# Kernel tuning notes

Hardware: AMD Instinct MI355X
Metric: run time of the kernel (lower is better)

Reference implementation:

```python
import jax, jax.numpy as jnp
import numpy as np

N_ROWS = 100000   # sparse matrix rows (nodes)
N_COLS = 8192     # input feature dim
UNITS = 128
NNZ = 2000000     # ~20 nonzeros per row


def setup_inputs() -> dict:
    key = jax.random.key(0)
    k1, k2, k3, k4, k5 = jax.random.split(key, 5)
    vals = jax.random.normal(k1, (NNZ,), dtype=jnp.float32)
    rows = jax.random.randint(k2, (NNZ,), 0, N_ROWS, dtype=jnp.int32)
    cols = jax.random.randint(k3, (NNZ,), 0, N_COLS, dtype=jnp.int32)
    # GlorotUniform-style scale for W, matching the TF initializer statistics
    limit = jnp.sqrt(6.0 / (N_COLS + UNITS)).astype(jnp.float32)
    W = jax.random.uniform(k4, (N_COLS, UNITS), dtype=jnp.float32, minval=-limit, maxval=limit)
    b = jax.random.uniform(k5, (UNITS,), dtype=jnp.float32, minval=-limit, maxval=limit)
    return {"vals": vals, "rows": rows, "cols": cols, "W": W, "b": b, "num_rows": N_ROWS}


def reference(vals, rows, cols, W, b, num_rows):
    # sparse (COO) [num_rows, F] @ dense W [F, units]:
    # gather the W row for each nonzero, scale by the nonzero value,
    # then scatter-add into the output row -> segment_sum over `rows`.
    gathered = W[cols] * vals[:, None]            # [nnz, units]
    out = jax.ops.segment_sum(gathered, rows, num_segments=num_rows)  # [num_rows, units]
    return out + b                                 # bias add (use_bias=True)
```

## Files before the change

### kernel.cpp

```cpp
#include <hip/hip_runtime.h>
#include <hip/hip_fp16.h>


#define UNITS 128
#define SCAN_BLK 1024
#define BROW 98
#define CBROW 784
#define NCC 128
#define CCAP 17664
#define CH3 4096
#define SLOTS 40
#define OVF_CAP 256
#define SPILL_CAP 8192


__global__ __launch_bounds__(512, 8) void partition_kernel(
        const float* __restrict__ vals, const int* __restrict__ rows,
        const int* __restrict__ cols, const float* __restrict__ W,
        __half2* __restrict__ Wh, int* __restrict__ ccur,
        float2* __restrict__ sortedA, float2* __restrict__ spill,
        int nnz, int nbcc, int wn2) {
    __shared__ float2 sStage[CH3];
    __shared__ unsigned char sBkt[CH3];
    __shared__ int hist[NCC];
    __shared__ int gdelta[NCC];

    const int t = threadIdx.x;
    const int lane = t & 63;
    const int w = t >> 6;
    const int bb = blockIdx.x;

    {
        const float2* W2 = (const float2*)W;
        int stride = gridDim.x * 512;
        for (int i = bb * 512 + t; i < wn2; i += stride)
            Wh[i] = __float22half2_rn(W2[i]);
    }

    const int chunk0 = bb * CH3;
    int n = nnz - chunk0;
    if (n > CH3) n = CH3;

    if (t < NCC) hist[t] = 0;
    __syncthreads();

    int rbuf[8];
#pragma unroll
    for (int j = 0; j < 8; ++j) {
        int r = j * 512 + t;
        int rv = -1;
        if (r < n) {
            rv = rows[chunk0 + r];
            atomicAdd(&hist[rv / CBROW], 1);
        }
        rbuf[j] = rv;
    }
    __syncthreads();

    if (w == 0) {
        int a0 = hist[2 * lane], a1 = hist[2 * lane + 1];
        int ps = a0 + a1;
        int inc = ps;
#pragma unroll
        for (int o = 1; o < 64; o <<= 1) {
            int u = __shfl_up(inc, o);
            if (lane >= o) inc += u;
        }
        int excl = inc - ps;
        int s0 = 2 * lane, s1 = 2 * lane + 1;
        int g0 = (s0 < nbcc && a0 > 0) ? atomicAdd(&ccur[s0 * 16], a0) : 0;
        int g1 = (s1 < nbcc && a1 > 0) ? atomicAdd(&ccur[s1 * 16], a1) : 0;
        gdelta[s0] = s0 * CCAP + g0 - excl;
        gdelta[s1] = s1 * CCAP + g1 - (excl + a0);
        hist[s0] = excl;
        hist[s1] = excl + a0;
    }
    __syncthreads();

#pragma unroll
    for (int j = 0; j < 8; ++j) {
        int rv = rbuf[j];
        if (rv >= 0) {
            int r = j * 512 + t;
            int bkt = rv / CBROW;
            int rlo = rv - bkt * CBROW;
            int pos = atomicAdd(&hist[bkt], 1);
            float v = vals[chunk0 + r];
            int col = cols[chunk0 + r];
            sStage[pos] = make_float2(v, __int_as_float(col | (rlo << 13)));
            sBkt[pos] = (unsigned char)bkt;
        }
    }
    __syncthreads();

    int* spill_cnt = &ccur[NCC * 16];
    for (int s = t; s < n; s += 512) {
        float2 e = sStage[s];
        int bkt = sBkt[s];
        int dest = gdelta[bkt] + s;
        if (dest < (bkt + 1) * CCAP) {
            sortedA[dest] = e;
        } else {
            int sp = atomicAdd(spill_cnt, 1);
            if (sp < SPILL_CAP) {
                int pk = __float_as_int(e.y);
                int row = bkt * CBROW + (pk >> 13);
                spill[sp] = make_float2(e.x, __int_as_float((pk & 8191) | (row << 13)));
            }
        }
    }
}


__global__ __launch_bounds__(512, 8) void fused_sort_compute_kernel(
        const float2* __restrict__ A, const int* __restrict__ ccur,
        const __half2* __restrict__ Wh, const float* __restrict__ b,
        float* __restrict__ out, const float2* __restrict__ spill, int NR) {
    __shared__ float2 st[BROW * SLOTS];
    __shared__ float2 ovf[OVF_CAP];
    __shared__ int cnt_s[BROW + 6];
    __shared__ int ovf_n;
    __shared__ int spill_n;
    const int t = threadIdx.x;
    const int lane = t & 63;
    const int w = t >> 6;

    const int nwg = gridDim.x;
    const int orig = blockIdx.x;
    const int q = nwg >> 3, r8 = nwg & 7, xcd = orig & 7, idx = orig >> 3;
    const int f = (xcd < r8 ? xcd * (q + 1) : r8 * (q + 1) + (xcd - r8) * q) + idx;

    const int c = f >> 3, sb = f & 7;
    const int r0 = f * BROW;
    const int rlo0 = sb * BROW;
    const size_t base = (size_t)c * CCAP;
    int segn = ccur[c * 16];
    if (segn > CCAP) segn = CCAP;

    const float2 bias = ((const float2*)b)[lane];

    if (t < BROW + 6) cnt_s[t] = 0;
    if (t == 0) {
        ovf_n = 0;
        int sn = ccur[NCC * 16];
        spill_n = (sn > SPILL_CAP) ? SPILL_CAP : sn;
    }
    for (int i = t; i < BROW * SLOTS; i += 512)
        st[i] = make_float2(0.f, __int_as_float(0));
    __syncthreads();

    const float4* A4 = (const float4*)(A + base);
    const int seg2 = segn >> 1;
    for (int k2 = t; k2 < seg2; k2 += 512) {
        float4 qv = A4[k2];
        {
            int pk = __float_as_int(qv.y);
            unsigned rl = (unsigned)(pk >> 13) - rlo0;
            if (rl < BROW) {
                int p = atomicAdd(&cnt_s[rl], 1);
                if (p < SLOTS) st[rl * SLOTS + p] = make_float2(qv.x, __int_as_float(pk & 8191));
                else {
                    int qn = atomicAdd(&ovf_n, 1);
                    if (qn < OVF_CAP) ovf[qn] = make_float2(qv.x, __int_as_float((pk & 8191) | (rl << 13)));
                }
            }
        }
        {
            int pk = __float_as_int(qv.w);
            unsigned rl = (unsigned)(pk >> 13) - rlo0;
            if (rl < BROW) {
                int p = atomicAdd(&cnt_s[rl], 1);
                if (p < SLOTS) st[rl * SLOTS + p] = make_float2(qv.z, __int_as_float(pk & 8191));
                else {
                    int qn = atomicAdd(&ovf_n, 1);
                    if (qn < OVF_CAP) ovf[qn] = make_float2(qv.z, __int_as_float((pk & 8191) | (rl << 13)));
                }
            }
        }
    }
    if ((segn & 1) && t == 0) {
        float2 e = A[base + segn - 1];
        int pk = __float_as_int(e.y);
        unsigned rl = (unsigned)(pk >> 13) - rlo0;
        if (rl < BROW) {
            int p = atomicAdd(&cnt_s[rl], 1);
            if (p < SLOTS) st[rl * SLOTS + p] = make_float2(e.x, __int_as_float(pk & 8191));
            else {
                int qn = atomicAdd(&ovf_n, 1);
                if (qn < OVF_CAP) ovf[qn] = make_float2(e.x, __int_as_float((pk & 8191) | (rl << 13)));
            }
        }
    }
    __syncthreads();

    const int on = (ovf_n > OVF_CAP) ? OVF_CAP : ovf_n;
    const int sn = spill_n;
    for (int rA = w; rA < BROW; rA += 16) {
        const int rB = rA + 8;
        const bool hasB = (rB < BROW);
        int cA = cnt_s[rA]; if (cA > SLOTS) cA = SLOTS;
        int cB = 0;
        if (hasB) { cB = cnt_s[rB]; if (cB > SLOTS) cB = SLOTS; }
        const float2* sA = &st[rA * SLOTS];
        const float2* sB = &st[(hasB ? rB : rA) * SLOTS];
        int m = (cA > cB) ? cA : cB;
        m = (m + 3) & ~3;
        float axA0 = 0.f, ayA0 = 0.f, axA1 = 0.f, ayA1 = 0.f;
        float axB0 = 0.f, ayB0 = 0.f, axB1 = 0.f, ayB1 = 0.f;
        for (int k = 0; k < m; k += 4) {
            float2 a0 = sA[k], a1 = sA[k + 1], a2 = sA[k + 2], a3 = sA[k + 3];
            float2 b0 = sB[k], b1 = sB[k + 1], b2 = sB[k + 2], b3 = sB[k + 3];
            int ca0 = __float_as_int(a0.y) & 8191;
            int ca1 = __float_as_int(a1.y) & 8191;
            int ca2 = __float_as_int(a2.y) & 8191;
            int ca3 = __float_as_int(a3.y) & 8191;
            int cb0 = __float_as_int(b0.y) & 8191;
            int cb1 = __float_as_int(b1.y) & 8191;
            int cb2 = __float_as_int(b2.y) & 8191;
            int cb3 = __float_as_int(b3.y) & 8191;
            float2 wa0 = __half22float2(Wh[ca0 * 64 + lane]);
            float2 wa1 = __half22float2(Wh[ca1 * 64 + lane]);
            float2 wa2 = __half22float2(Wh[ca2 * 64 + lane]);
            float2 wa3 = __half22float2(Wh[ca3 * 64 + lane]);
            float2 wb0 = __half22float2(Wh[cb0 * 64 + lane]);
            float2 wb1 = __half22float2(Wh[cb1 * 64 + lane]);
            float2 wb2 = __half22float2(Wh[cb2 * 64 + lane]);
            float2 wb3 = __half22float2(Wh[cb3 * 64 + lane]);
            axA0 += a0.x * wa0.x; ayA0 += a0.x * wa0.y;
            axA1 += a1.x * wa1.x; ayA1 += a1.x * wa1.y;
            axA0 += a2.x * wa2.x; ayA0 += a2.x * wa2.y;
            axA1 += a3.x * wa3.x; ayA1 += a3.x * wa3.y;
            axB0 += b0.x * wb0.x; ayB0 += b0.x * wb0.y;
            axB1 += b1.x * wb1.x; ayB1 += b1.x * wb1.y;
            axB0 += b2.x * wb2.x; ayB0 += b2.x * wb2.y;
            axB1 += b3.x * wb3.x; ayB1 += b3.x * wb3.y;
        }
        {
            int grow = r0 + rA;
            if (grow < NR) {
                for (int q2 = 0; q2 < on; ++q2) {
                    float2 eo = ovf[q2];
                    int pk = __float_as_int(eo.y);
                    if ((pk >> 13) == rA) {
                        float2 wv = __half22float2(Wh[(pk & 8191) * 64 + lane]);
                        axA0 += eo.x * wv.x; ayA0 += eo.x * wv.y;
                    }
                }
                for (int s2 = 0; s2 < sn; ++s2) {
                    float2 es = spill[s2];
                    int pk = __float_as_int(es.y);
                    if ((pk >> 13) == grow) {
                        float2 wv = __half22float2(Wh[(pk & 8191) * 64 + lane]);
                        axA0 += es.x * wv.x; ayA0 += es.x * wv.y;
                    }
                }
                ((float2*)out)[(size_t)grow * 64 + lane] =
                    make_float2(axA0 + axA1 + bias.x, ayA0 + ayA1 + bias.y);
            }
        }
        if (hasB) {
            int grow = r0 + rB;
            if (grow < NR) {
                for (int q2 = 0; q2 < on; ++q2) {
                    float2 eo = ovf[q2];
                    int pk = __float_as_int(eo.y);
                    if ((pk >> 13) == rB) {
                        float2 wv = __half22float2(Wh[(pk & 8191) * 64 + lane]);
                        axB0 += eo.x * wv.x; ayB0 += eo.x * wv.y;
                    }
                }
                for (int s2 = 0; s2 < sn; ++s2) {
                    float2 es = spill[s2];
                    int pk = __float_as_int(es.y);
                    if ((pk >> 13) == grow) {
                        float2 wv = __half22float2(Wh[(pk & 8191) * 64 + lane]);
                        axB0 += es.x * wv.x; ayB0 += es.x * wv.y;
                    }
                }
                ((float2*)out)[(size_t)grow * 64 + lane] =
                    make_float2(axB0 + axB1 + bias.x, ayB0 + ayB1 + bias.y);
            }
        }
    }
}


__global__ void hist_kernel(const int* __restrict__ rows, int* __restrict__ counts, int nnz) {
    int i = blockIdx.x * blockDim.x + threadIdx.x;
    if (i < nnz) atomicAdd(&counts[rows[i]], 1);
}

__global__ void scan1_kernel(const int* __restrict__ counts, int* __restrict__ tmp,
                             int* __restrict__ bsums, int NR, int NS) {
    __shared__ int s[SCAN_BLK];
    int t = threadIdx.x;
    int i = blockIdx.x * SCAN_BLK + t;
    int x = (i < NR) ? counts[i] : 0;
    s[t] = x;
    __syncthreads();
    for (int off = 1; off < SCAN_BLK; off <<= 1) {
        int v = (t >= off) ? s[t - off] : 0;
        __syncthreads();
        s[t] += v;
        __syncthreads();
    }
    if (i < NS) tmp[i] = s[t] - x;
    if (t == SCAN_BLK - 1) bsums[blockIdx.x] = s[SCAN_BLK - 1];
}

__global__ void scan2_kernel(int* __restrict__ bsums, int nb) {
    if (threadIdx.x == 0 && blockIdx.x == 0) {
        int run = 0;
        for (int i = 0; i < nb; ++i) { int c = bsums[i]; bsums[i] = run; run += c; }
    }
}

__global__ void scan3_kernel(const int* __restrict__ tmp, const int* __restrict__ bsums,
                             int* __restrict__ row_start, int* __restrict__ cursor,
                             int NR, int NS) {
    int i = blockIdx.x * blockDim.x + threadIdx.x;
    if (i < NS) {
        int v = tmp[i] + bsums[i >> 10];
        row_start[i] = v;
        if (i < NR) cursor[i] = v;
    }
}

__global__ void scatter_sort_kernel(const float* __restrict__ vals, const int* __restrict__ rows,
                                    const int* __restrict__ cols, int* __restrict__ cursor,
                                    float2* __restrict__ sorted, int nnz) {
    int i = blockIdx.x * blockDim.x + threadIdx.x;
    if (i < nnz) {
        int r = rows[i];
        int p = atomicAdd(&cursor[r], 1);
        sorted[p] = make_float2(vals[i], __int_as_float(cols[i]));
    }
}

__global__ void compute_kernel(const float2* __restrict__ sorted, const int* __restrict__ row_start,
                               const float* __restrict__ W, const float* __restrict__ b,
                               float* __restrict__ out, int NR) {
    int lane = threadIdx.x & 63;
    int wv = threadIdx.x >> 6;
    int row = blockIdx.x * 4 + wv;
    if (row >= NR) return;
    int start = row_start[row];
    int end   = row_start[row + 1];
    const float2* W2 = (const float2*)W;
    float accx0 = 0.f, accy0 = 0.f, accx1 = 0.f, accy1 = 0.f;
    for (int base = start; base < end; base += 64) {
        int m = end - base;
        if (m > 64) m = 64;
        float2 p = make_float2(0.f, __int_as_float(0));
        if (lane < m) p = sorted[base + lane];
        int vi = __float_as_int(p.x);
        int ci = __float_as_int(p.y);
        int rounds = (m + 3) & ~3;
        for (int j = 0; j < rounds; j += 4) {
            float v0 = __int_as_float(__builtin_amdgcn_readlane(vi, j));
            int   c0 = __builtin_amdgcn_readlane(ci, j);
            float v1 = __int_as_float(__builtin_amdgcn_readlane(vi, j + 1));
            int   c1 = __builtin_amdgcn_readlane(ci, j + 1);
            float v2 = __int_as_float(__builtin_amdgcn_readlane(vi, j + 2));
            int   c2 = __builtin_amdgcn_readlane(ci, j + 2);
            float v3 = __int_as_float(__builtin_amdgcn_readlane(vi, j + 3));
            int   c3 = __builtin_amdgcn_readlane(ci, j + 3);
            float2 w0 = W2[c0 * 64 + lane];
            float2 w1 = W2[c1 * 64 + lane];
            float2 w2 = W2[c2 * 64 + lane];
            float2 w3 = W2[c3 * 64 + lane];
            accx0 += v0 * w0.x; accy0 += v0 * w0.y;
            accx1 += v1 * w1.x; accy1 += v1 * w1.y;
            accx0 += v2 * w2.x; accy0 += v2 * w2.y;
            accx1 += v3 * w3.x; accy1 += v3 * w3.y;
        }
    }
    float2 bb = ((const float2*)b)[lane];
    ((float2*)out)[(size_t)row * 64 + lane] =
        make_float2(accx0 + accx1 + bb.x, accy0 + accy1 + bb.y);
}


__global__ void init_bias_kernel(float* __restrict__ out, const float* __restrict__ b, int total4) {
    const float4* b4 = (const float4*)b;
    float4* out4 = (float4*)out;
    int stride = gridDim.x * blockDim.x;
    for (int j = blockIdx.x * blockDim.x + threadIdx.x; j < total4; j += stride)
        out4[j] = b4[j & 31];
}

__global__ void scatter_atomic_kernel(const float* __restrict__ vals, const int* __restrict__ rows,
                                      const int* __restrict__ cols, const float* __restrict__ W,
                                      float* __restrict__ out, int nnz) {
    long long idx = (long long)blockIdx.x * blockDim.x + threadIdx.x;
    int i = (int)(idx >> 5);
    int c = (int)(idx & 31);
    if (i >= nnz) return;
    int row = rows[i], col = cols[i];
    float v = vals[i];
    float4 w = ((const float4*)W)[col * 32 + c];
    float* o = out + (size_t)row * UNITS + (c << 2);
    atomicAdd(o + 0, v * w.x);
    atomicAdd(o + 1, v * w.y);
    atomicAdd(o + 2, v * w.z);
    atomicAdd(o + 3, v * w.w);
}

extern "C" void kernel_launch(void* const* d_in, const int* in_sizes, int n_in,
                              void* d_out, int out_size, void* d_ws, size_t ws_size,
                              hipStream_t stream) {
    const float* vals = (const float*)d_in[0];
    const int*   rows = (const int*)d_in[1];
    const int*   cols = (const int*)d_in[2];
    const float* W    = (const float*)d_in[3];
    const float* b    = (const float*)d_in[4];
    float* out = (float*)d_out;

    const int nnz = in_sizes[0];
    const int NW  = in_sizes[3];
    const int NR  = out_size / UNITS;
    const int NS  = NR + 1;
    const int NB  = (NS + SCAN_BLK - 1) / SCAN_BLK;
    const int nbf  = (NR + BROW - 1) / BROW;
    const int nbcc = (NR + CBROW - 1) / CBROW;

    auto align = [](size_t x) { return (x + 255) & ~(size_t)255; };

    size_t off_ccur    = 0;
    size_t off_wh      = align(off_ccur + (size_t)(NCC * 16 + 1) * 4);
    size_t off_sortedA = align(off_wh + (size_t)NW * 2);
    size_t off_spill   = align(off_sortedA + (size_t)NCC * CCAP * 8);
    size_t needed_full = off_spill + (size_t)SPILL_CAP * 8;

    size_t t2_counts   = 0;
    size_t t2_tmp      = align(t2_counts + (size_t)NR * 4);
    size_t t2_bsums    = align(t2_tmp    + (size_t)NS * 4);
    size_t t2_rowstart = align(t2_bsums  + (size_t)NB * 4);
    size_t t2_cursor   = align(t2_rowstart + (size_t)NS * 4);
    size_t t2_sorted   = align(t2_cursor + (size_t)NR * 4);
    size_t needed_r2   = t2_sorted + (size_t)nnz * 8;

    char* ws = (char*)d_ws;

    if (ws_size >= needed_full && nbcc >= 1 && nbcc <= NCC && NR >= 1) {
        int*     ccur    = (int*)(ws + off_ccur);
        __half2* Wh      = (__half2*)(ws + off_wh);
        float2*  sortedA = (float2*)(ws + off_sortedA);
        float2*  spill   = (float2*)(ws + off_spill);

        hipMemsetAsync(ccur, 0, (size_t)(NCC * 16 + 1) * 4, stream);
        {
            int grid = (nnz + CH3 - 1) / CH3;
            partition_kernel<<<grid, 512, 0, stream>>>(vals, rows, cols, W, Wh,
                                                       ccur, sortedA, spill,
                                                       nnz, nbcc, NW / 2);
        }
        fused_sort_compute_kernel<<<nbf, 512, 0, stream>>>(sortedA, ccur, Wh, b,
                                                           out, spill, NR);
    } else if (ws_size >= needed_r2) {
        int*    counts    = (int*)(ws + t2_counts);
        int*    tmp       = (int*)(ws + t2_tmp);
        int*    bsums     = (int*)(ws + t2_bsums);
        int*    row_start = (int*)(ws + t2_rowstart);
        int*    cursor    = (int*)(ws + t2_cursor);
        float2* sorted    = (float2*)(ws + t2_sorted);

        hipMemsetAsync(counts, 0, (size_t)NR * 4, stream);
        {
            int block = 256, grid = (nnz + block - 1) / block;
            hist_kernel<<<grid, block, 0, stream>>>(rows, counts, nnz);
        }
        scan1_kernel<<<NB, SCAN_BLK, 0, stream>>>(counts, tmp, bsums, NR, NS);
        scan2_kernel<<<1, 64, 0, stream>>>(bsums, NB);
        {
            int block = 256, grid = (NS + block - 1) / block;
            scan3_kernel<<<grid, block, 0, stream>>>(tmp, bsums, row_start, cursor, NR, NS);
        }
        {
            int block = 256, grid = (nnz + block - 1) / block;
            scatter_sort_kernel<<<grid, block, 0, stream>>>(vals, rows, cols, cursor, sorted, nnz);
        }
        {
            int grid = (NR + 3) / 4;
            compute_kernel<<<grid, 256, 0, stream>>>(sorted, row_start, W, b, out, NR);
        }
    } else {
        int total4 = out_size / 4;
        int block = 256;
        int grid = (total4 + block - 1) / block;
        init_bias_kernel<<<grid, block, 0, stream>>>(out, b, total4);
        long long total_threads = (long long)nnz * 32;
        long long g2 = (total_threads + block - 1) / block;
        scatter_atomic_kernel<<<(int)g2, block, 0, stream>>>(vals, rows, cols, W, out, nnz);
    }
}
```

Before: 156.5 us.

## Use fixed per-chunk bucket slots with sentinel padding instead of global atomic offsets

The partition kernel no longer reserves space in each bucket's segment with a global atomicAdd. Each (bucket, chunk) pair now owns a fixed slot range of PER entries in sortedA, and unused slots are filled with a sentinel row that the consumer ignores. Entries beyond PER go to a per-bucket overflow segment that the compute kernel also scans, and the global spill list with its per-row rescan is gone. This removes inter-block atomic contention and the spill scan, but the consumer now reads a padded segment (nch*PER entries per bucket, roughly double the real count) and the partition kernel writes extra padding.

Result: faster. 150.6 us (-3.8%).

```diff
diff --git a/kernel.cpp b/kernel.cpp
--- a/kernel.cpp
+++ b/kernel.cpp
@@ -7,23 +7,25 @@
 #define BROW 98
 #define CBROW 784
 #define NCC 128
-#define CCAP 17664
 #define CH3 4096
+#define PER 40
+#define OCAP 1024
 #define SLOTS 40
 #define OVF_CAP 256
-#define SPILL_CAP 8192
+#define SENT (1023 << 13)
 
 
 __global__ __launch_bounds__(512, 8) void partition_kernel(
         const float* __restrict__ vals, const int* __restrict__ rows,
         const int* __restrict__ cols, const float* __restrict__ W,
-        __half2* __restrict__ Wh, int* __restrict__ ccur,
-        float2* __restrict__ sortedA, float2* __restrict__ spill,
-        int nnz, int nbcc, int wn2) {
+        __half2* __restrict__ Wh, int* __restrict__ ocur,
+        float2* __restrict__ sortedA, float2* __restrict__ ovfseg,
+        int nnz, int nbcc, int nch, int wn2) {
     __shared__ float2 sStage[CH3];
     __shared__ unsigned char sBkt[CH3];
     __shared__ int hist[NCC];
-    __shared__ int gdelta[NCC];
+    __shared__ int excl[NCC];
+    __shared__ int cnt[NCC];
 
     const int t = threadIdx.x;
     const int lane = t & 63;
@@ -66,14 +68,10 @@
             int u = __shfl_up(inc, o);
             if (lane >= o) inc += u;
         }
-        int excl = inc - ps;
-        int s0 = 2 * lane, s1 = 2 * lane + 1;
-        int g0 = (s0 < nbcc && a0 > 0) ? atomicAdd(&ccur[s0 * 16], a0) : 0;
-        int g1 = (s1 < nbcc && a1 > 0) ? atomicAdd(&ccur[s1 * 16], a1) : 0;
-        gdelta[s0] = s0 * CCAP + g0 - excl;
-        gdelta[s1] = s1 * CCAP + g1 - (excl + a0);
-        hist[s0] = excl;
-        hist[s1] = excl + a0;
+        int e0 = inc - ps;
+        cnt[2 * lane] = a0;  cnt[2 * lane + 1] = a1;
+        excl[2 * lane] = e0; excl[2 * lane + 1] = e0 + a0;
+        hist[2 * lane] = e0; hist[2 * lane + 1] = e0 + a0;
     }
     __syncthreads();
 
@@ -93,34 +91,39 @@
     }
     __syncthreads();
 
-    int* spill_cnt = &ccur[NCC * 16];
+    const size_t rowsz = (size_t)nch * PER;
     for (int s = t; s < n; s += 512) {
         float2 e = sStage[s];
         int bkt = sBkt[s];
-        int dest = gdelta[bkt] + s;
-        if (dest < (bkt + 1) * CCAP) {
-            sortedA[dest] = e;
+        int local = s - excl[bkt];
+        if (local < PER) {
+            sortedA[(size_t)bkt * rowsz + (size_t)bb * PER + local] = e;
         } else {
-            int sp = atomicAdd(spill_cnt, 1);
-            if (sp < SPILL_CAP) {
-                int pk = __float_as_int(e.y);
-                int row = bkt * CBROW + (pk >> 13);
-                spill[sp] = make_float2(e.x, __int_as_float((pk & 8191) | (row << 13)));
-            }
+            int o = atomicAdd(&ocur[bkt * 16], 1);
+            if (o < OCAP) ovfseg[bkt * OCAP + o] = e;
+        }
+    }
+    for (int u = t; u < NCC * PER; u += 512) {
+        int bkt = u / PER, sl = u - bkt * PER;
+        if (bkt < nbcc) {
+            int cb = cnt[bkt]; if (cb > PER) cb = PER;
+            if (sl >= cb)
+                sortedA[(size_t)bkt * rowsz + (size_t)bb * PER + sl] =
+                    make_float2(0.f, __int_as_float(SENT));
         }
     }
 }
 
 
 __global__ __launch_bounds__(512, 8) void fused_sort_compute_kernel(
-        const float2* __restrict__ A, const int* __restrict__ ccur,
-        const __half2* __restrict__ Wh, const float* __restrict__ b,
-        float* __restrict__ out, const float2* __restrict__ spill, int NR) {
+        const float2* __restrict__ A, const int* __restrict__ ocur,
+        const float2* __restrict__ ovfseg, const __half2* __restrict__ Wh,
+        const float* __restrict__ b, float* __restrict__ out,
+        int nchPER, int NR) {
     __shared__ float2 st[BROW * SLOTS];
     __shared__ float2 ovf[OVF_CAP];
     __shared__ int cnt_s[BROW + 6];
     __shared__ int ovf_n;
-    __shared__ int spill_n;
     const int t = threadIdx.x;
     const int lane = t & 63;
     const int w = t >> 6;
@@ -133,24 +136,18 @@
     const int c = f >> 3, sb = f & 7;
     const int r0 = f * BROW;
     const int rlo0 = sb * BROW;
-    const size_t base = (size_t)c * CCAP;
-    int segn = ccur[c * 16];
-    if (segn > CCAP) segn = CCAP;
+    const size_t base = (size_t)c * nchPER;
 
     const float2 bias = ((const float2*)b)[lane];
 
     if (t < BROW + 6) cnt_s[t] = 0;
-    if (t == 0) {
-        ovf_n = 0;
-        int sn = ccur[NCC * 16];
-        spill_n = (sn > SPILL_CAP) ? SPILL_CAP : sn;
-    }
+    if (t == 0) ovf_n = 0;
     for (int i = t; i < BROW * SLOTS; i += 512)
         st[i] = make_float2(0.f, __int_as_float(0));
     __syncthreads();
 
     const float4* A4 = (const float4*)(A + base);
-    const int seg2 = segn >> 1;
+    const int seg2 = nchPER >> 1;
     for (int k2 = t; k2 < seg2; k2 += 512) {
         float4 qv = A4[k2];
         {
@@ -178,23 +175,26 @@
             }
         }
     }
-    if ((segn & 1) && t == 0) {
-        float2 e = A[base + segn - 1];
-        int pk = __float_as_int(e.y);
-        unsigned rl = (unsigned)(pk >> 13) - rlo0;
-        if (rl < BROW) {
-            int p = atomicAdd(&cnt_s[rl], 1);
-            if (p < SLOTS) st[rl * SLOTS + p] = make_float2(e.x, __int_as_float(pk & 8191));
-            else {
-                int qn = atomicAdd(&ovf_n, 1);
-                if (qn < OVF_CAP) ovf[qn] = make_float2(e.x, __int_as_float((pk & 8191) | (rl << 13)));
+    {
+        int on0 = ocur[c * 16];
+        if (on0 > OCAP) on0 = OCAP;
+        for (int k = t; k < on0; k += 512) {
+            float2 e = ovfseg[c * OCAP + k];
+            int pk = __float_as_int(e.y);
+            unsigned rl = (unsigned)(pk >> 13) - rlo0;
+            if (rl < BROW) {
+                int p = atomicAdd(&cnt_s[rl], 1);
+                if (p < SLOTS) st[rl * SLOTS + p] = make_float2(e.x, __int_as_float(pk & 8191));
+                else {
+                    int qn = atomicAdd(&ovf_n, 1);
+                    if (qn < OVF_CAP) ovf[qn] = make_float2(e.x, __int_as_float((pk & 8191) | (rl << 13)));
+                }
             }
         }
     }
     __syncthreads();
 
     const int on = (ovf_n > OVF_CAP) ? OVF_CAP : ovf_n;
-    const int sn = spill_n;
     for (int rA = w; rA < BROW; rA += 16) {
         const int rB = rA + 8;
         const bool hasB = (rB < BROW);
@@ -246,14 +246,6 @@
                         axA0 += eo.x * wv.x; ayA0 += eo.x * wv.y;
                     }
                 }
-                for (int s2 = 0; s2 < sn; ++s2) {
-                    float2 es = spill[s2];
-                    int pk = __float_as_int(es.y);
-                    if ((pk >> 13) == grow) {
-                        float2 wv = __half22float2(Wh[(pk & 8191) * 64 + lane]);
-                        axA0 += es.x * wv.x; ayA0 += es.x * wv.y;
-                    }
-                }
                 ((float2*)out)[(size_t)grow * 64 + lane] =
                     make_float2(axA0 + axA1 + bias.x, ayA0 + ayA1 + bias.y);
             }
@@ -267,14 +259,6 @@
                     if ((pk >> 13) == rB) {
                         float2 wv = __half22float2(Wh[(pk & 8191) * 64 + lane]);
                         axB0 += eo.x * wv.x; ayB0 += eo.x * wv.y;
-                    }
-                }
-                for (int s2 = 0; s2 < sn; ++s2) {
-                    float2 es = spill[s2];
-                    int pk = __float_as_int(es.y);
-                    if ((pk >> 13) == grow) {
-                        float2 wv = __half22float2(Wh[(pk & 8191) * 64 + lane]);
-                        axB0 += es.x * wv.x; ayB0 += es.x * wv.y;
                     }
                 }
                 ((float2*)out)[(size_t)grow * 64 + lane] =
@@ -423,14 +407,16 @@
     const int NB  = (NS + SCAN_BLK - 1) / SCAN_BLK;
     const int nbf  = (NR + BROW - 1) / BROW;
     const int nbcc = (NR + CBROW - 1) / CBROW;
+    const int nch  = (nnz + CH3 - 1) / CH3;
+    const int nchPER = nch * PER;
 
     auto align = [](size_t x) { return (x + 255) & ~(size_t)255; };
 
-    size_t off_ccur    = 0;
-    size_t off_wh      = align(off_ccur + (size_t)(NCC * 16 + 1) * 4);
+    size_t off_ocur    = 0;
+    size_t off_wh      = align(off_ocur + (size_t)NCC * 16 * 4);
     size_t off_sortedA = align(off_wh + (size_t)NW * 2);
-    size_t off_spill   = align(off_sortedA + (size_t)NCC * CCAP * 8);
-    size_t needed_full = off_spill + (size_t)SPILL_CAP * 8;
+    size_t off_ovf     = align(off_sortedA + (size_t)nbcc * (size_t)nchPER * 8);
+    size_t needed_full = off_ovf + (size_t)NCC * OCAP * 8;
 
     size_t t2_counts   = 0;
     size_t t2_tmp      = align(t2_counts + (size_t)NR * 4);
@@ -442,21 +428,18 @@
 
     char* ws = (char*)d_ws;
 
-    if (ws_size >= needed_full && nbcc >= 1 && nbcc <= NCC && NR >= 1) {
-        int*     ccur    = (int*)(ws + off_ccur);
+    if (ws_size >= needed_full && nbcc >= 1 && nbcc <= NCC && nch >= 1 && NR >= 1) {
+        int*     ocur    = (int*)(ws + off_ocur);
         __half2* Wh      = (__half2*)(ws + off_wh);
         float2*  sortedA = (float2*)(ws + off_sortedA);
-        float2*  spill   = (float2*)(ws + off_spill);
-
-        hipMemsetAsync(ccur, 0, (size_t)(NCC * 16 + 1) * 4, stream);
-        {
-            int grid = (nnz + CH3 - 1) / CH3;
-            partition_kernel<<<grid, 512, 0, stream>>>(vals, rows, cols, W, Wh,
-                                                       ccur, sortedA, spill,
-                                                       nnz, nbcc, NW / 2);
-        }
-        fused_sort_compute_kernel<<<nbf, 512, 0, stream>>>(sortedA, ccur, Wh, b,
-                                                           out, spill, NR);
+        float2*  ovfseg  = (float2*)(ws + off_ovf);
+
+        hipMemsetAsync(ocur, 0, (size_t)NCC * 16 * 4, stream);
+        partition_kernel<<<nch, 512, 0, stream>>>(vals, rows, cols, W, Wh,
+                                                  ocur, sortedA, ovfseg,
+                                                  nnz, nbcc, nch, NW / 2);
+        fused_sort_compute_kernel<<<nbf, 512, 0, stream>>>(sortedA, ocur, ovfseg,
+                                                           Wh, b, out, nchPER, NR);
     } else if (ws_size >= needed_r2) {
         int*    counts    = (int*)(ws + t2_counts);
         int*    tmp       = (int*)(ws + t2_tmp);
```
